# Kernel tuning notes

Hardware: AMD Instinct MI355X
Metric: run time of the kernel (lower is better)

Reference implementation:

```python
import jax, jax.numpy as jnp
import numpy as np

N, E = 50000, 640000          # nodes, edges
F_IN, HID, CLS = 128, 128, 64  # feature dims


def setup_inputs() -> dict:
    key = jax.random.key(0)
    ks = jax.random.split(key, 12)
    x = jax.random.normal(ks[0], (N, F_IN), dtype=jnp.float32)
    edge_index = jax.random.randint(ks[1], (2, E), 0, N, dtype=jnp.int32)
    s_in = 1.0 / np.sqrt(F_IN)
    s_h = 1.0 / np.sqrt(HID)
    return {
        "x": x,
        "edge_index": edge_index,
        "W0": jax.random.normal(ks[2], (F_IN, HID), jnp.float32) * s_in,
        "b0": jnp.zeros((HID,), jnp.float32),
        "W1": jax.random.normal(ks[3], (HID, HID), jnp.float32) * s_h,
        "b1": jnp.zeros((HID,), jnp.float32),
        "W2": jax.random.normal(ks[4], (HID, HID), jnp.float32) * s_h,
        "b2": jnp.zeros((HID,), jnp.float32),
        "W_lin": jax.random.normal(ks[5], (HID, CLS), jnp.float32) * s_h,
        "b_lin": jnp.zeros((CLS,), jnp.float32),
    }


def reference(x, edge_index, W0, b0, W1, b1, W2, b2, W_lin, b_lin):
    # GCNConv (PyG defaults): out = D^-1/2 (A + I) D^-1/2 (x @ W) + b
    row, col = edge_index[0], edge_index[1]  # source -> target
    # degree with self-loop (graph is fixed across layers, compute norms once)
    deg = jnp.zeros((N,), x.dtype).at[col].add(1.0) + 1.0
    dinv = jax.lax.rsqrt(deg)                 # deg >= 1, safe
    enorm = (dinv[row] * dinv[col])[:, None]  # [E,1] edge norm
    snorm = (dinv * dinv)[:, None]            # [N,1] self-loop norm

    def conv(h, W, b):
        h = h @ W                                             # [N,HID]
        agg = jnp.zeros_like(h).at[col].add(h[row] * enorm)   # neighbor agg
        return agg + h * snorm + b                            # + self loop + bias

    h = jax.nn.relu(conv(x, W0, b0))
    h = jax.nn.relu(conv(h, W1, b1))
    h = jax.nn.relu(conv(h, W2, b2))
    return h @ W_lin + b_lin
```

## Files before the change

kernel.cpp:

```cpp
#include <hip/hip_runtime.h>
#include <hip/hip_fp16.h>

#define N_NODES 50000
#define HID 128
#define CLS 64

#define NBINS 196
#define NBLK 256
#define LBUF_CAP 4096
#define WTOT 57344
#define GEMM0_BLOCKS 782

typedef __attribute__((ext_vector_type(8))) _Float16 f16x8;
typedef __attribute__((ext_vector_type(4))) float f32x4;

__global__ __launch_bounds__(256) void hist_wsplit_kernel(
    const int* __restrict__ col, int* __restrict__ hist,
    const float* __restrict__ W0, const float* __restrict__ W1,
    const float* __restrict__ W2, const float* __restrict__ Wl,
    __half* __restrict__ o0h, __half* __restrict__ o0l,
    __half* __restrict__ o1h, __half* __restrict__ o1l,
    __half* __restrict__ o2h, __half* __restrict__ o2l,
    __half* __restrict__ o3h, __half* __restrict__ o3l,
    int E, int chunk) {
    int widx = blockIdx.x * 256 + threadIdx.x;
    if (widx < WTOT) {
        const float* W;
        __half *oh, *ol;
        int NCdim, local;
        if (widx < 16384)      { W = W0; oh = o0h; ol = o0l; NCdim = 128; local = widx; }
        else if (widx < 32768) { W = W1; oh = o1h; ol = o1l; NCdim = 128; local = widx - 16384; }
        else if (widx < 49152) { W = W2; oh = o2h; ol = o2l; NCdim = 128; local = widx - 32768; }
        else                   { W = Wl; oh = o3h; ol = o3l; NCdim = 64;  local = widx - 49152; }
        int nn = local >> 7;
        int k = local & 127;
        float v = W[(size_t)k * NCdim + nn];
        __half h = __float2half_rn(v);
        oh[local] = h;
        ol[local] = __float2half_rn(v - __half2float(h));
    }
    __shared__ int h[NBINS];
    for (int i = threadIdx.x; i < NBINS; i += 256) h[i] = 0;
    __syncthreads();
    int b = blockIdx.x;
    int beg = b * chunk;
    int end = min(E, beg + chunk);
    if (beg < end) {
        int vend = beg + ((end - beg) & ~3);
        for (int i = beg + threadIdx.x * 4; i < vend; i += 1024) {
            int4 c4 = *(const int4*)(col + i);
            atomicAdd(&h[c4.x >> 8], 1);
            atomicAdd(&h[c4.y >> 8], 1);
            atomicAdd(&h[c4.z >> 8], 1);
            atomicAdd(&h[c4.w >> 8], 1);
        }
        int i = vend + threadIdx.x;
        if (i < end) atomicAdd(&h[col[i] >> 8], 1);
    }
    __syncthreads();
    for (int i = threadIdx.x; i < NBINS; i += 256)
        hist[i * NBLK + b] = h[i];
}

__global__ __launch_bounds__(256) void scatter_kernel(
    const int* __restrict__ row, const int* __restrict__ col,
    const int* __restrict__ hist, int* __restrict__ binBase_g,
    int* __restrict__ sbuf_src, unsigned char* __restrict__ sbuf_c,
    int E, int chunk) {
    __shared__ int sTot[256];
    __shared__ int cur[NBINS];
    int b = blockIdx.x, t = threadIdx.x;
    int partial = 0, total = 0;
    if (t < NBINS) {
        const int4* r4 = (const int4*)(hist + t * NBLK);
        int nb4 = b >> 2, rem = b & 3;
        for (int j = 0; j < NBLK / 4; ++j) {
            int4 v = r4[j];
            int s = v.x + v.y + v.z + v.w;
            total += s;
            if (j < nb4) partial += s;
            else if (j == nb4) {
                if (rem > 0) partial += v.x;
                if (rem > 1) partial += v.y;
                if (rem > 2) partial += v.z;
            }
        }
    }
    sTot[t] = (t < NBINS) ? total : 0;
    __syncthreads();
#pragma unroll
    for (int off = 1; off < 256; off <<= 1) {
        int u = (t >= off) ? sTot[t - off] : 0;
        __syncthreads();
        sTot[t] += u;
        __syncthreads();
    }
    int myBase = sTot[t] - total;
    if (t < NBINS) cur[t] = myBase + partial;
    if (b == 0) {
        if (t < NBINS) binBase_g[t] = myBase;
        if (t == 0) binBase_g[NBINS] = E;
    }
    __syncthreads();
    int beg = b * chunk;
    int end = min(E, beg + chunk);
    if (beg >= end) return;
    int vend = beg + ((end - beg) & ~3);
    for (int i = beg + t * 4; i < vend; i += 1024) {
        int4 c4 = *(const int4*)(col + i);
        int4 r4 = *(const int4*)(row + i);
        int p;
        p = atomicAdd(&cur[c4.x >> 8], 1); sbuf_src[p] = r4.x; sbuf_c[p] = (unsigned char)(c4.x & 255);
        p = atomicAdd(&cur[c4.y >> 8], 1); sbuf_src[p] = r4.y; sbuf_c[p] = (unsigned char)(c4.y & 255);
        p = atomicAdd(&cur[c4.z >> 8], 1); sbuf_src[p] = r4.z; sbuf_c[p] = (unsigned char)(c4.z & 255);
        p = atomicAdd(&cur[c4.w >> 8], 1); sbuf_src[p] = r4.w; sbuf_c[p] = (unsigned char)(c4.w & 255);
    }
    int i = vend + t;
    if (i < end) {
        int c = col[i];
        int p = atomicAdd(&cur[c >> 8], 1);
        sbuf_src[p] = row[i];
        sbuf_c[p] = (unsigned char)(c & 255);
    }
}

template<int NC, bool ADD_BIAS, bool HALF_OUT, bool F32A>
__device__ __forceinline__ void gemm_body(
    const void* __restrict__ Av, const __half* __restrict__ Bh,
    const __half* __restrict__ Bl, const float* __restrict__ bias,
    void* __restrict__ Cv, int M, int rowTile) {
    constexpr int NT = NC / 16;
    int lane = threadIdx.x & 63;
    int m0 = rowTile << 4;
    if (m0 >= M) return;
    int mr = lane & 15;
    int kq = (lane >> 4) << 3;

    const __half* ah = F32A ? nullptr : (const __half*)Av + (size_t)(m0 + mr) * 128 + kq;
    const float*  af = F32A ? (const float*)Av + (size_t)(m0 + mr) * 128 + kq : nullptr;
    const __half* bh = Bh + (size_t)mr * 128 + kq;
    const __half* bl = Bl + (size_t)mr * 128 + kq;

    f32x4 acc[NT];
#pragma unroll
    for (int t = 0; t < NT; ++t) acc[t] = (f32x4){0.f, 0.f, 0.f, 0.f};

#pragma unroll
    for (int kc = 0; kc < 128; kc += 32) {
        f16x8 a;
        if (F32A) {
            float4 lo = *(const float4*)(af + kc);
            float4 hi = *(const float4*)(af + kc + 4);
            a[0] = (_Float16)lo.x; a[1] = (_Float16)lo.y;
            a[2] = (_Float16)lo.z; a[3] = (_Float16)lo.w;
            a[4] = (_Float16)hi.x; a[5] = (_Float16)hi.y;
            a[6] = (_Float16)hi.z; a[7] = (_Float16)hi.w;
        } else {
            a = *(const f16x8*)(ah + kc);
        }
#pragma unroll
        for (int t = 0; t < NT; ++t) {
            f16x8 wh = *(const f16x8*)(bh + (size_t)t * 16 * 128 + kc);
            f16x8 wl = *(const f16x8*)(bl + (size_t)t * 16 * 128 + kc);
            acc[t] = __builtin_amdgcn_mfma_f32_16x16x32_f16(a, wh, acc[t], 0, 0, 0);
            acc[t] = __builtin_amdgcn_mfma_f32_16x16x32_f16(a, wl, acc[t], 0, 0, 0);
        }
    }

    int r0 = m0 + ((lane >> 4) << 2);
    int cc = lane & 15;
#pragma unroll
    for (int t = 0; t < NT; ++t) {
        float bsv = ADD_BIAS ? bias[t * 16 + cc] : 0.f;
#pragma unroll
        for (int r = 0; r < 4; ++r) {
            float val = acc[t][r] + bsv;
            size_t idx = (size_t)(r0 + r) * NC + t * 16 + cc;
            if (HALF_OUT)
                ((__half*)Cv)[idx] = __float2half_rn(val);
            else
                ((float*)Cv)[idx] = val;
        }
    }
}

template<int NC, bool ADD_BIAS, bool HALF_OUT, bool F32A>
__global__ __launch_bounds__(256) void mfma_gemm_f16(
    const void* __restrict__ Av, const __half* __restrict__ Bh,
    const __half* __restrict__ Bl, const float* __restrict__ bias,
    void* __restrict__ Cv, int M) {
    gemm_body<NC, ADD_BIAS, HALF_OUT, F32A>(Av, Bh, Bl, bias, Cv, M,
                                            blockIdx.x * 4 + (threadIdx.x >> 6));
}

__global__ __launch_bounds__(256) void csrplace_gemm0_kernel(
    const int* __restrict__ binBase,
    const int* __restrict__ sbuf_src, const unsigned char* __restrict__ sbuf_c,
    float* __restrict__ dinv, int* __restrict__ row_ptr, int* __restrict__ csr_src,
    const float* __restrict__ x, const __half* __restrict__ W0h,
    const __half* __restrict__ W0l, __half* __restrict__ h2, int n, int E) {
    __shared__ int lcnt[256];
    __shared__ int lcur[256];
    __shared__ int ss[256];
    __shared__ int lbuf[LBUF_CAP];
    int b = blockIdx.x;
    if (b >= NBINS) {
        gemm_body<128, false, true, true>(x, W0h, W0l, nullptr, h2, n,
                                          (b - NBINS) * 4 + (threadIdx.x >> 6));
        return;
    }
    int t = threadIdx.x;
    lcnt[t] = 0;
    __syncthreads();
    int beg = binBase[b], end = binBase[b + 1];
    for (int j = beg + t; j < end; j += 256)
        atomicAdd(&lcnt[sbuf_c[j]], 1);
    __syncthreads();
    int deg = lcnt[t];
    int node = b * 256 + t;
    if (node < n) dinv[node] = rsqrtf((float)deg + 1.0f);
    ss[t] = deg;
    __syncthreads();
#pragma unroll
    for (int off = 1; off < 256; off <<= 1) {
        int u = (t >= off) ? ss[t - off] : 0;
        __syncthreads();
        ss[t] += u;
        __syncthreads();
    }
    int excl = ss[t] - deg;
    lcur[t] = excl;
    int total = ss[255];
    if (node < n) row_ptr[node] = beg + excl;
    if (b == 0 && t == 0) row_ptr[n] = E;
    __syncthreads();
    for (int j = beg + t; j < end; j += 256) {
        int c = sbuf_c[j];
        int pos = atomicAdd(&lcur[c], 1);
        lbuf[pos] = sbuf_src[j];
    }
    __syncthreads();
    for (int j = t; j < total; j += 256) csr_src[beg + j] = lbuf[j];
}

__global__ __launch_bounds__(256) void agg_kernel(
    const __half* __restrict__ h2, const int* __restrict__ row_ptr,
    const int* __restrict__ csr_src, const float* __restrict__ dinv,
    const float* __restrict__ bias, __half* __restrict__ outA, int n) {
    int wid = (blockIdx.x * 256 + threadIdx.x) >> 6;
    int lane = threadIdx.x & 63;
    if (wid >= n) return;
    int beg = row_ptr[wid];
    int end = row_ptr[wid + 1];
    float dv = dinv[wid];
    float ax = 0.f, ay = 0.f;
    int loff = lane << 1;
    for (int base = beg; base < end; base += 64) {
        int cnt = end - base;
        if (cnt > 64) cnt = 64;
        int msrc = 0;
        float mw = 0.f;
        if (lane < cnt) {
            msrc = csr_src[base + lane];
            mw = dinv[msrc] * dv;
        }
        int j = 0;
        for (; j + 8 <= cnt; j += 8) {
            int s0 = __shfl(msrc, j),     s1 = __shfl(msrc, j + 1);
            int s2 = __shfl(msrc, j + 2), s3 = __shfl(msrc, j + 3);
            int s4 = __shfl(msrc, j + 4), s5 = __shfl(msrc, j + 5);
            int s6 = __shfl(msrc, j + 6), s7 = __shfl(msrc, j + 7);
            float w0 = __shfl(mw, j),     w1 = __shfl(mw, j + 1);
            float w2 = __shfl(mw, j + 2), w3 = __shfl(mw, j + 3);
            float w4 = __shfl(mw, j + 4), w5 = __shfl(mw, j + 5);
            float w6 = __shfl(mw, j + 6), w7 = __shfl(mw, j + 7);
            float2 v0 = __half22float2(*(const __half2*)(h2 + ((size_t)s0 << 7) + loff));
            float2 v1 = __half22float2(*(const __half2*)(h2 + ((size_t)s1 << 7) + loff));
            float2 v2 = __half22float2(*(const __half2*)(h2 + ((size_t)s2 << 7) + loff));
            float2 v3 = __half22float2(*(const __half2*)(h2 + ((size_t)s3 << 7) + loff));
            float2 v4 = __half22float2(*(const __half2*)(h2 + ((size_t)s4 << 7) + loff));
            float2 v5 = __half22float2(*(const __half2*)(h2 + ((size_t)s5 << 7) + loff));
            float2 v6 = __half22float2(*(const __half2*)(h2 + ((size_t)s6 << 7) + loff));
            float2 v7 = __half22float2(*(const __half2*)(h2 + ((size_t)s7 << 7) + loff));
            ax = fmaf(v0.x, w0, ax); ay = fmaf(v0.y, w0, ay);
            ax = fmaf(v1.x, w1, ax); ay = fmaf(v1.y, w1, ay);
            ax = fmaf(v2.x, w2, ax); ay = fmaf(v2.y, w2, ay);
            ax = fmaf(v3.x, w3, ax); ay = fmaf(v3.y, w3, ay);
            ax = fmaf(v4.x, w4, ax); ay = fmaf(v4.y, w4, ay);
            ax = fmaf(v5.x, w5, ax); ay = fmaf(v5.y, w5, ay);
            ax = fmaf(v6.x, w6, ax); ay = fmaf(v6.y, w6, ay);
            ax = fmaf(v7.x, w7, ax); ay = fmaf(v7.y, w7, ay);
        }
        for (; j + 4 <= cnt; j += 4) {
            int s0 = __shfl(msrc, j),     s1 = __shfl(msrc, j + 1);
            int s2 = __shfl(msrc, j + 2), s3 = __shfl(msrc, j + 3);
            float w0 = __shfl(mw, j),     w1 = __shfl(mw, j + 1);
            float w2 = __shfl(mw, j + 2), w3 = __shfl(mw, j + 3);
            float2 v0 = __half22float2(*(const __half2*)(h2 + ((size_t)s0 << 7) + loff));
            float2 v1 = __half22float2(*(const __half2*)(h2 + ((size_t)s1 << 7) + loff));
            float2 v2 = __half22float2(*(const __half2*)(h2 + ((size_t)s2 << 7) + loff));
            float2 v3 = __half22float2(*(const __half2*)(h2 + ((size_t)s3 << 7) + loff));
            ax = fmaf(v0.x, w0, ax); ay = fmaf(v0.y, w0, ay);
            ax = fmaf(v1.x, w1, ax); ay = fmaf(v1.y, w1, ay);
            ax = fmaf(v2.x, w2, ax); ay = fmaf(v2.y, w2, ay);
            ax = fmaf(v3.x, w3, ax); ay = fmaf(v3.y, w3, ay);
        }
        for (; j < cnt; ++j) {
            int s = __shfl(msrc, j);
            float w = __shfl(mw, j);
            float2 v = __half22float2(*(const __half2*)(h2 + ((size_t)s << 7) + loff));
            ax = fmaf(v.x, w, ax); ay = fmaf(v.y, w, ay);
        }
    }
    float sn = dv * dv;
    float2 self = __half22float2(*(const __half2*)(h2 + ((size_t)wid << 7) + loff));
    float2 b = *(const float2*)(bias + loff);
    float ox = fmaxf(fmaf(self.x, sn, ax) + b.x, 0.f);
    float oy = fmaxf(fmaf(self.y, sn, ay) + b.y, 0.f);
    *(__half2*)(outA + ((size_t)wid << 7) + loff) = __float22half2_rn(make_float2(ox, oy));
}

extern "C" void kernel_launch(void* const* d_in, const int* in_sizes, int n_in,
                              void* d_out, int out_size, void* d_ws, size_t ws_size,
                              hipStream_t stream) {
    const float* x  = (const float*)d_in[0];
    const int* ei   = (const int*)d_in[1];
    const float* W0 = (const float*)d_in[2];
    const float* b0 = (const float*)d_in[3];
    const float* W1 = (const float*)d_in[4];
    const float* b1 = (const float*)d_in[5];
    const float* W2 = (const float*)d_in[6];
    const float* b2 = (const float*)d_in[7];
    const float* Wl = (const float*)d_in[8];
    const float* bl = (const float*)d_in[9];
    float* out = (float*)d_out;

    const int N = N_NODES;
    const int E = in_sizes[1] / 2;
    const int* row = ei;
    const int* col = ei + E;
    const int chunk = (((E + NBLK - 1) / NBLK) + 3) & ~3;

    char* ws = (char*)d_ws;
    auto alloc = [&](size_t bytes) {
        char* p = ws;
        ws += (bytes + 255) & ~(size_t)255;
        return p;
    };
    int*   hist    = (int*)alloc((size_t)NBINS * NBLK * 4);
    int*   binBase = (int*)alloc((size_t)(NBINS + 1) * 4);
    int*   sbuf_src= (int*)alloc((size_t)E * 4);
    unsigned char* sbuf_c = (unsigned char*)alloc((size_t)E);
    int*   row_ptr = (int*)alloc((size_t)(N + 1) * 4);
    float* dinv    = (float*)alloc((size_t)N * 4);
    int*   csr_src = (int*)alloc((size_t)E * 4);
    __half* h2     = (__half*)alloc((size_t)N * HID * 2);
    __half* hA     = (__half*)alloc((size_t)N * HID * 2);
    __half* Wt_h[4];
    __half* Wt_l[4];
    for (int i = 0; i < 3; ++i) {
        Wt_h[i] = (__half*)alloc((size_t)HID * HID * 2);
        Wt_l[i] = (__half*)alloc((size_t)HID * HID * 2);
    }
    Wt_h[3] = (__half*)alloc((size_t)CLS * HID * 2);
    Wt_l[3] = (__half*)alloc((size_t)CLS * HID * 2);

    hist_wsplit_kernel<<<NBLK, 256, 0, stream>>>(col, hist, W0, W1, W2, Wl,
        Wt_h[0], Wt_l[0], Wt_h[1], Wt_l[1], Wt_h[2], Wt_l[2], Wt_h[3], Wt_l[3], E, chunk);
    scatter_kernel<<<NBLK, 256, 0, stream>>>(row, col, hist, binBase, sbuf_src, sbuf_c, E, chunk);
    csrplace_gemm0_kernel<<<NBINS + GEMM0_BLOCKS, 256, 0, stream>>>(
        binBase, sbuf_src, sbuf_c, dinv, row_ptr, csr_src,
        x, Wt_h[0], Wt_l[0], h2, N, E);

    const int gemmBlocks = GEMM0_BLOCKS;
    const int aggBlocks  = (N + 3) / 4;

    agg_kernel<<<aggBlocks, 256, 0, stream>>>(h2, row_ptr, csr_src, dinv, b0, hA, N);
    mfma_gemm_f16<128, false, true, false><<<gemmBlocks, 256, 0, stream>>>(hA, Wt_h[1], Wt_l[1], nullptr, h2, N);
    agg_kernel<<<aggBlocks, 256, 0, stream>>>(h2, row_ptr, csr_src, dinv, b1, hA, N);
    mfma_gemm_f16<128, false, true, false><<<gemmBlocks, 256, 0, stream>>>(hA, Wt_h[2], Wt_l[2], nullptr, h2, N);
    agg_kernel<<<aggBlocks, 256, 0, stream>>>(h2, row_ptr, csr_src, dinv, b2, hA, N);
    mfma_gemm_f16<64, true, false, false><<<gemmBlocks, 256, 0, stream>>>(hA, Wt_h[3], Wt_l[3], bl, out, N);
}
```

Measured before the change: 318.2 us.

## Fuse neighbor aggregation with following GEMM via shared-memory row tile

Each layer's aggregation kernel and the following MFMA GEMM are merged into one kernel. A block aggregates 16 node rows (4 per wave) into an LDS tile, then the four waves split the output column tiles of the GEMM against that tile. This removes the round trip of the intermediate activation through global memory and three kernel launches. In exchange each block does more serial aggregation work before the GEMM, occupancy changes, and the weight fragments are reloaded per block.

```diff
diff --git a/kernel.cpp b/kernel.cpp
--- a/kernel.cpp
+++ b/kernel.cpp
@@ -10,6 +10,7 @@
 #define LBUF_CAP 4096
 #define WTOT 57344
 #define GEMM0_BLOCKS 782
+#define AROW 136
 
 typedef __attribute__((ext_vector_type(8))) _Float16 f16x8;
 typedef __attribute__((ext_vector_type(4))) float f32x4;
@@ -124,40 +125,32 @@
     }
 }
 
-template<int NC, bool ADD_BIAS, bool HALF_OUT, bool F32A>
-__device__ __forceinline__ void gemm_body(
-    const void* __restrict__ Av, const __half* __restrict__ Bh,
-    const __half* __restrict__ Bl, const float* __restrict__ bias,
-    void* __restrict__ Cv, int M, int rowTile) {
-    constexpr int NT = NC / 16;
+__device__ __forceinline__ void gemm0_body(
+    const float* __restrict__ x, const __half* __restrict__ Bh,
+    const __half* __restrict__ Bl, __half* __restrict__ C, int M, int rowTile) {
+    constexpr int NT = 8;
     int lane = threadIdx.x & 63;
     int m0 = rowTile << 4;
     if (m0 >= M) return;
     int mr = lane & 15;
     int kq = (lane >> 4) << 3;
 
-    const __half* ah = F32A ? nullptr : (const __half*)Av + (size_t)(m0 + mr) * 128 + kq;
-    const float*  af = F32A ? (const float*)Av + (size_t)(m0 + mr) * 128 + kq : nullptr;
+    const float*  af = x + (size_t)(m0 + mr) * 128 + kq;
     const __half* bh = Bh + (size_t)mr * 128 + kq;
     const __half* bl = Bl + (size_t)mr * 128 + kq;
 
     f32x4 acc[NT];
 #pragma unroll
     for (int t = 0; t < NT; ++t) acc[t] = (f32x4){0.f, 0.f, 0.f, 0.f};
-
 #pragma unroll
     for (int kc = 0; kc < 128; kc += 32) {
+        float4 lo = *(const float4*)(af + kc);
+        float4 hi = *(const float4*)(af + kc + 4);
         f16x8 a;
-        if (F32A) {
-            float4 lo = *(const float4*)(af + kc);
-            float4 hi = *(const float4*)(af + kc + 4);
-            a[0] = (_Float16)lo.x; a[1] = (_Float16)lo.y;
-            a[2] = (_Float16)lo.z; a[3] = (_Float16)lo.w;
-            a[4] = (_Float16)hi.x; a[5] = (_Float16)hi.y;
-            a[6] = (_Float16)hi.z; a[7] = (_Float16)hi.w;
-        } else {
-            a = *(const f16x8*)(ah + kc);
-        }
+        a[0] = (_Float16)lo.x; a[1] = (_Float16)lo.y;
+        a[2] = (_Float16)lo.z; a[3] = (_Float16)lo.w;
+        a[4] = (_Float16)hi.x; a[5] = (_Float16)hi.y;
+        a[6] = (_Float16)hi.z; a[7] = (_Float16)hi.w;
 #pragma unroll
         for (int t = 0; t < NT; ++t) {
             f16x8 wh = *(const f16x8*)(bh + (size_t)t * 16 * 128 + kc);
@@ -166,31 +159,14 @@
             acc[t] = __builtin_amdgcn_mfma_f32_16x16x32_f16(a, wl, acc[t], 0, 0, 0);
         }
     }
-
     int r0 = m0 + ((lane >> 4) << 2);
     int cc = lane & 15;
 #pragma unroll
-    for (int t = 0; t < NT; ++t) {
-        float bsv = ADD_BIAS ? bias[t * 16 + cc] : 0.f;
-#pragma unroll
-        for (int r = 0; r < 4; ++r) {
-            float val = acc[t][r] + bsv;
-            size_t idx = (size_t)(r0 + r) * NC + t * 16 + cc;
-            if (HALF_OUT)
-                ((__half*)Cv)[idx] = __float2half_rn(val);
-            else
-                ((float*)Cv)[idx] = val;
-        }
-    }
-}
-
-template<int NC, bool ADD_BIAS, bool HALF_OUT, bool F32A>
-__global__ __launch_bounds__(256) void mfma_gemm_f16(
-    const void* __restrict__ Av, const __half* __restrict__ Bh,
-    const __half* __restrict__ Bl, const float* __restrict__ bias,
-    void* __restrict__ Cv, int M) {
-    gemm_body<NC, ADD_BIAS, HALF_OUT, F32A>(Av, Bh, Bl, bias, Cv, M,
-                                            blockIdx.x * 4 + (threadIdx.x >> 6));
+    for (int t = 0; t < NT; ++t)
+#pragma unroll
+        for (int r = 0; r < 4; ++r)
+            C[(size_t)(r0 + r) * 128 + t * 16 + cc] =
+                __float2half_rn(acc[t][r]);
 }
 
 __global__ __launch_bounds__(256) void csrplace_gemm0_kernel(
@@ -205,8 +181,7 @@
     __shared__ int lbuf[LBUF_CAP];
     int b = blockIdx.x;
     if (b >= NBINS) {
-        gemm_body<128, false, true, true>(x, W0h, W0l, nullptr, h2, n,
-                                          (b - NBINS) * 4 + (threadIdx.x >> 6));
+        gemm0_body(x, W0h, W0l, h2, n, (b - NBINS) * 4 + (threadIdx.x >> 6));
         return;
     }
     int t = threadIdx.x;
@@ -243,81 +218,133 @@
     for (int j = t; j < total; j += 256) csr_src[beg + j] = lbuf[j];
 }
 
-__global__ __launch_bounds__(256) void agg_kernel(
+template<int NC, bool HEAD>
+__global__ __launch_bounds__(256) void agg_gemm_kernel(
     const __half* __restrict__ h2, const int* __restrict__ row_ptr,
     const int* __restrict__ csr_src, const float* __restrict__ dinv,
-    const float* __restrict__ bias, __half* __restrict__ outA, int n) {
-    int wid = (blockIdx.x * 256 + threadIdx.x) >> 6;
+    const float* __restrict__ bias,
+    const __half* __restrict__ Bh, const __half* __restrict__ Bl,
+    const float* __restrict__ gbias, void* __restrict__ Cv, int n) {
+    __shared__ __half Als[16][AROW];
+    int wave = threadIdx.x >> 6;
     int lane = threadIdx.x & 63;
-    if (wid >= n) return;
-    int beg = row_ptr[wid];
-    int end = row_ptr[wid + 1];
-    float dv = dinv[wid];
-    float ax = 0.f, ay = 0.f;
     int loff = lane << 1;
-    for (int base = beg; base < end; base += 64) {
-        int cnt = end - base;
-        if (cnt > 64) cnt = 64;
-        int msrc = 0;
-        float mw = 0.f;
-        if (lane < cnt) {
-            msrc = csr_src[base + lane];
-            mw = dinv[msrc] * dv;
-        }
-        int j = 0;
-        for (; j + 8 <= cnt; j += 8) {
-            int s0 = __shfl(msrc, j),     s1 = __shfl(msrc, j + 1);
-            int s2 = __shfl(msrc, j + 2), s3 = __shfl(msrc, j + 3);
-            int s4 = __shfl(msrc, j + 4), s5 = __shfl(msrc, j + 5);
-            int s6 = __shfl(msrc, j + 6), s7 = __shfl(msrc, j + 7);
-            float w0 = __shfl(mw, j),     w1 = __shfl(mw, j + 1);
-            float w2 = __shfl(mw, j + 2), w3 = __shfl(mw, j + 3);
-            float w4 = __shfl(mw, j + 4), w5 = __shfl(mw, j + 5);
-            float w6 = __shfl(mw, j + 6), w7 = __shfl(mw, j + 7);
-            float2 v0 = __half22float2(*(const __half2*)(h2 + ((size_t)s0 << 7) + loff));
-            float2 v1 = __half22float2(*(const __half2*)(h2 + ((size_t)s1 << 7) + loff));
-            float2 v2 = __half22float2(*(const __half2*)(h2 + ((size_t)s2 << 7) + loff));
-            float2 v3 = __half22float2(*(const __half2*)(h2 + ((size_t)s3 << 7) + loff));
-            float2 v4 = __half22float2(*(const __half2*)(h2 + ((size_t)s4 << 7) + loff));
-            float2 v5 = __half22float2(*(const __half2*)(h2 + ((size_t)s5 << 7) + loff));
-            float2 v6 = __half22float2(*(const __half2*)(h2 + ((size_t)s6 << 7) + loff));
-            float2 v7 = __half22float2(*(const __half2*)(h2 + ((size_t)s7 << 7) + loff));
-            ax = fmaf(v0.x, w0, ax); ay = fmaf(v0.y, w0, ay);
-            ax = fmaf(v1.x, w1, ax); ay = fmaf(v1.y, w1, ay);
-            ax = fmaf(v2.x, w2, ax); ay = fmaf(v2.y, w2, ay);
-            ax = fmaf(v3.x, w3, ax); ay = fmaf(v3.y, w3, ay);
-            ax = fmaf(v4.x, w4, ax); ay = fmaf(v4.y, w4, ay);
-            ax = fmaf(v5.x, w5, ax); ay = fmaf(v5.y, w5, ay);
-            ax = fmaf(v6.x, w6, ax); ay = fmaf(v6.y, w6, ay);
-            ax = fmaf(v7.x, w7, ax); ay = fmaf(v7.y, w7, ay);
-        }
-        for (; j + 4 <= cnt; j += 4) {
-            int s0 = __shfl(msrc, j),     s1 = __shfl(msrc, j + 1);
-            int s2 = __shfl(msrc, j + 2), s3 = __shfl(msrc, j + 3);
-            float w0 = __shfl(mw, j),     w1 = __shfl(mw, j + 1);
-            float w2 = __shfl(mw, j + 2), w3 = __shfl(mw, j + 3);
-            float2 v0 = __half22float2(*(const __half2*)(h2 + ((size_t)s0 << 7) + loff));
-            float2 v1 = __half22float2(*(const __half2*)(h2 + ((size_t)s1 << 7) + loff));
-            float2 v2 = __half22float2(*(const __half2*)(h2 + ((size_t)s2 << 7) + loff));
-            float2 v3 = __half22float2(*(const __half2*)(h2 + ((size_t)s3 << 7) + loff));
-            ax = fmaf(v0.x, w0, ax); ay = fmaf(v0.y, w0, ay);
-            ax = fmaf(v1.x, w1, ax); ay = fmaf(v1.y, w1, ay);
-            ax = fmaf(v2.x, w2, ax); ay = fmaf(v2.y, w2, ay);
-            ax = fmaf(v3.x, w3, ax); ay = fmaf(v3.y, w3, ay);
-        }
-        for (; j < cnt; ++j) {
-            int s = __shfl(msrc, j);
-            float w = __shfl(mw, j);
-            float2 v = __half22float2(*(const __half2*)(h2 + ((size_t)s << 7) + loff));
-            ax = fmaf(v.x, w, ax); ay = fmaf(v.y, w, ay);
-        }
-    }
-    float sn = dv * dv;
-    float2 self = __half22float2(*(const __half2*)(h2 + ((size_t)wid << 7) + loff));
-    float2 b = *(const float2*)(bias + loff);
-    float ox = fmaxf(fmaf(self.x, sn, ax) + b.x, 0.f);
-    float oy = fmaxf(fmaf(self.y, sn, ay) + b.y, 0.f);
-    *(__half2*)(outA + ((size_t)wid << 7) + loff) = __float22half2_rn(make_float2(ox, oy));
+    int m0 = blockIdx.x << 4;
+
+#pragma unroll
+    for (int k = 0; k < 4; ++k) {
+        int lr = wave * 4 + k;
+        int wid = m0 + lr;
+        if (wid >= n) break;
+        int beg = row_ptr[wid];
+        int end = row_ptr[wid + 1];
+        float dv = dinv[wid];
+        float ax = 0.f, ay = 0.f;
+        for (int base = beg; base < end; base += 64) {
+            int cnt = end - base;
+            if (cnt > 64) cnt = 64;
+            int msrc = 0;
+            float mw = 0.f;
+            if (lane < cnt) {
+                msrc = csr_src[base + lane];
+                mw = dinv[msrc] * dv;
+            }
+            int j = 0;
+            for (; j + 8 <= cnt; j += 8) {
+                int s0 = __shfl(msrc, j),     s1 = __shfl(msrc, j + 1);
+                int s2 = __shfl(msrc, j + 2), s3 = __shfl(msrc, j + 3);
+                int s4 = __shfl(msrc, j + 4), s5 = __shfl(msrc, j + 5);
+                int s6 = __shfl(msrc, j + 6), s7 = __shfl(msrc, j + 7);
+                float w0 = __shfl(mw, j),     w1 = __shfl(mw, j + 1);
+                float w2 = __shfl(mw, j + 2), w3 = __shfl(mw, j + 3);
+                float w4 = __shfl(mw, j + 4), w5 = __shfl(mw, j + 5);
+                float w6 = __shfl(mw, j + 6), w7 = __shfl(mw, j + 7);
+                float2 v0 = __half22float2(*(const __half2*)(h2 + ((size_t)s0 << 7) + loff));
+                float2 v1 = __half22float2(*(const __half2*)(h2 + ((size_t)s1 << 7) + loff));
+                float2 v2 = __half22float2(*(const __half2*)(h2 + ((size_t)s2 << 7) + loff));
+                float2 v3 = __half22float2(*(const __half2*)(h2 + ((size_t)s3 << 7) + loff));
+                float2 v4 = __half22float2(*(const __half2*)(h2 + ((size_t)s4 << 7) + loff));
+                float2 v5 = __half22float2(*(const __half2*)(h2 + ((size_t)s5 << 7) + loff));
+                float2 v6 = __half22float2(*(const __half2*)(h2 + ((size_t)s6 << 7) + loff));
+                float2 v7 = __half22float2(*(const __half2*)(h2 + ((size_t)s7 << 7) + loff));
+                ax = fmaf(v0.x, w0, ax); ay = fmaf(v0.y, w0, ay);
+                ax = fmaf(v1.x, w1, ax); ay = fmaf(v1.y, w1, ay);
+                ax = fmaf(v2.x, w2, ax); ay = fmaf(v2.y, w2, ay);
+                ax = fmaf(v3.x, w3, ax); ay = fmaf(v3.y, w3, ay);
+                ax = fmaf(v4.x, w4, ax); ay = fmaf(v4.y, w4, ay);
+                ax = fmaf(v5.x, w5, ax); ay = fmaf(v5.y, w5, ay);
+                ax = fmaf(v6.x, w6, ax); ay = fmaf(v6.y, w6, ay);
+                ax = fmaf(v7.x, w7, ax); ay = fmaf(v7.y, w7, ay);
+            }
+            for (; j + 4 <= cnt; j += 4) {
+                int s0 = __shfl(msrc, j),     s1 = __shfl(msrc, j + 1);
+                int s2 = __shfl(msrc, j + 2), s3 = __shfl(msrc, j + 3);
+                float w0 = __shfl(mw, j),     w1 = __shfl(mw, j + 1);
+                float w2 = __shfl(mw, j + 2), w3 = __shfl(mw, j + 3);
+                float2 v0 = __half22float2(*(const __half2*)(h2 + ((size_t)s0 << 7) + loff));
+                float2 v1 = __half22float2(*(const __half2*)(h2 + ((size_t)s1 << 7) + loff));
+                float2 v2 = __half22float2(*(const __half2*)(h2 + ((size_t)s2 << 7) + loff));
+                float2 v3 = __half22float2(*(const __half2*)(h2 + ((size_t)s3 << 7) + loff));
+                ax = fmaf(v0.x, w0, ax); ay = fmaf(v0.y, w0, ay);
+                ax = fmaf(v1.x, w1, ax); ay = fmaf(v1.y, w1, ay);
+                ax = fmaf(v2.x, w2, ax); ay = fmaf(v2.y, w2, ay);
+                ax = fmaf(v3.x, w3, ax); ay = fmaf(v3.y, w3, ay);
+            }
+            for (; j < cnt; ++j) {
+                int s = __shfl(msrc, j);
+                float w = __shfl(mw, j);
+                float2 v = __half22float2(*(const __half2*)(h2 + ((size_t)s << 7) + loff));
+                ax = fmaf(v.x, w, ax); ay = fmaf(v.y, w, ay);
+            }
+        }
+        float sn = dv * dv;
+        float2 self = __half22float2(*(const __half2*)(h2 + ((size_t)wid << 7) + loff));
+        float2 b = *(const float2*)(bias + loff);
+        float ox = fmaxf(fmaf(self.x, sn, ax) + b.x, 0.f);
+        float oy = fmaxf(fmaf(self.y, sn, ay) + b.y, 0.f);
+        *(__half2*)&Als[lr][loff] = __float22half2_rn(make_float2(ox, oy));
+    }
+    __syncthreads();
+
+    constexpr int NT = NC / 16;
+    constexpr int TPW = NT / 4;
+    int mr = lane & 15;
+    int kq = (lane >> 4) << 3;
+    const __half* bh = Bh + (size_t)mr * 128 + kq;
+    const __half* bl = Bl + (size_t)mr * 128 + kq;
+
+    f32x4 acc[TPW];
+#pragma unroll
+    for (int t = 0; t < TPW; ++t) acc[t] = (f32x4){0.f, 0.f, 0.f, 0.f};
+#pragma unroll
+    for (int kc = 0; kc < 128; kc += 32) {
+        f16x8 a = *(const f16x8*)&Als[mr][kq + kc];
+#pragma unroll
+        for (int t = 0; t < TPW; ++t) {
+            int tile = wave * TPW + t;
+            f16x8 wh = *(const f16x8*)(bh + (size_t)tile * 16 * 128 + kc);
+            f16x8 wl = *(const f16x8*)(bl + (size_t)tile * 16 * 128 + kc);
+            acc[t] = __builtin_amdgcn_mfma_f32_16x16x32_f16(a, wh, acc[t], 0, 0, 0);
+            acc[t] = __builtin_amdgcn_mfma_f32_16x16x32_f16(a, wl, acc[t], 0, 0, 0);
+        }
+    }
+    int r0 = m0 + ((lane >> 4) << 2);
+    int cc = lane & 15;
+#pragma unroll
+    for (int t = 0; t < TPW; ++t) {
+        int tile = wave * TPW + t;
+        float bsv = HEAD ? gbias[tile * 16 + cc] : 0.f;
+#pragma unroll
+        for (int r = 0; r < 4; ++r) {
+            if (r0 + r >= n) break;
+            size_t idx = (size_t)(r0 + r) * NC + tile * 16 + cc;
+            float val = acc[t][r] + bsv;
+            if (HEAD)
+                ((float*)Cv)[idx] = val;
+            else
+                ((__half*)Cv)[idx] = __float2half_rn(val);
+        }
+    }
 }
 
 extern "C" void kernel_launch(void* const* d_in, const int* in_sizes, int n_in,
@@ -354,8 +381,8 @@
     int*   row_ptr = (int*)alloc((size_t)(N + 1) * 4);
     float* dinv    = (float*)alloc((size_t)N * 4);
     int*   csr_src = (int*)alloc((size_t)E * 4);
-    __half* h2     = (__half*)alloc((size_t)N * HID * 2);
-    __half* hA     = (__half*)alloc((size_t)N * HID * 2);
+    __half* h2a    = (__half*)alloc((size_t)N * HID * 2);
+    __half* h2b    = (__half*)alloc((size_t)N * HID * 2);
     __half* Wt_h[4];
     __half* Wt_l[4];
     for (int i = 0; i < 3; ++i) {
@@ -370,15 +397,14 @@
     scatter_kernel<<<NBLK, 256, 0, stream>>>(row, col, hist, binBase, sbuf_src, sbuf_c, E, chunk);
     csrplace_gemm0_kernel<<<NBINS + GEMM0_BLOCKS, 256, 0, stream>>>(
         binBase, sbuf_src, sbuf_c, dinv, row_ptr, csr_src,
-        x, Wt_h[0], Wt_l[0], h2, N, E);
-
-    const int gemmBlocks = GEMM0_BLOCKS;
-    const int aggBlocks  = (N + 3) / 4;
-
-    agg_kernel<<<aggBlocks, 256, 0, stream>>>(h2, row_ptr, csr_src, dinv, b0, hA, N);
-    mfma_gemm_f16<128, false, true, false><<<gemmBlocks, 256, 0, stream>>>(hA, Wt_h[1], Wt_l[1], nullptr, h2, N);
-    agg_kernel<<<aggBlocks, 256, 0, stream>>>(h2, row_ptr, csr_src, dinv, b1, hA, N);
-    mfma_gemm_f16<128, false, true, false><<<gemmBlocks, 256, 0, stream>>>(hA, Wt_h[2], Wt_l[2], nullptr, h2, N);
-    agg_kernel<<<aggBlocks, 256, 0, stream>>>(h2, row_ptr, csr_src, dinv, b2, hA, N);
-    mfma_gemm_f16<64, true, false, false><<<gemmBlocks, 256, 0, stream>>>(hA, Wt_h[3], Wt_l[3], bl, out, N);
-}
+        x, Wt_h[0], Wt_l[0], h2a, N, E);
+
+    const int fusedBlocks = (N + 15) / 16;
+
+    agg_gemm_kernel<128, false><<<fusedBlocks, 256, 0, stream>>>(
+        h2a, row_ptr, csr_src, dinv, b0, Wt_h[1], Wt_l[1], nullptr, h2b, N);
+    agg_gemm_kernel<128, false><<<fusedBlocks, 256, 0, stream>>>(
+        h2b, row_ptr, csr_src, dinv, b1, Wt_h[2], Wt_l[2], nullptr, h2a, N);
+    agg_gemm_kernel<64, true><<<fusedBlocks, 256, 0, stream>>>(
+        h2a, row_ptr, csr_src, dinv, b2, Wt_h[3], Wt_l[3], bl, out, N);
+}
```

New measurement: 281.0 us. -11.7%, faster.
